# Kernel tuning notes

Hardware: AMD Instinct MI355X
Metric: run time of the kernel (lower is better)

The kernel has to match this reference:

```python
import jax, jax.numpy as jnp
import numpy as np

D_MODEL = 1024
N_HEADS = 16
D_K = D_MODEL // N_HEADS
SCALE = float(np.sqrt(D_K))


def setup_inputs() -> dict:
    key = jax.random.key(0)
    ks = jax.random.split(key, 12)
    B, S = 2, 2048
    std = 1.0 / np.sqrt(D_MODEL)
    inp = {
        "query": jax.random.normal(ks[0], (B, S, D_MODEL), jnp.float32),
        "key": jax.random.normal(ks[1], (B, S, D_MODEL), jnp.float32),
        "value": jax.random.normal(ks[2], (B, S, D_MODEL), jnp.float32),
        "mask": jnp.ones((B, S), jnp.int32),
        "Wq": jax.random.normal(ks[3], (D_MODEL, D_MODEL), jnp.float32) * std,
        "bq": jnp.zeros((D_MODEL,), jnp.float32),
        "Wk": jax.random.normal(ks[4], (D_MODEL, D_MODEL), jnp.float32) * std,
        "bk": jnp.zeros((D_MODEL,), jnp.float32),
        "Wv": jax.random.normal(ks[5], (D_MODEL, D_MODEL), jnp.float32) * std,
        "bv": jnp.zeros((D_MODEL,), jnp.float32),
        "Wo": jax.random.normal(ks[6], (D_MODEL, D_MODEL), jnp.float32) * std,
        "bo": jnp.zeros((D_MODEL,), jnp.float32),
    }
    return inp


def reference(query, key, value, mask, Wq, bq, Wk, bk, Wv, bv, Wo, bo):
    B, S, _ = query.shape
    # projections -> [B, H, S, d_k]
    def proj(x, W, b):
        return (x @ W.T + b).reshape(B, S, N_HEADS, D_K).transpose(0, 2, 1, 3)

    Q = proj(query, Wq, bq)
    K = proj(key, Wk, bk)
    V = proj(value, Wv, bv)
    # [B, H, Sq, Sk] scores
    scores = jnp.einsum("bhqd,bhkd->bhqk", Q, K) / SCALE
    m = mask[:, None, None, :]  # broadcast over heads and query positions
    scores = jnp.where(m == 0, jnp.float32(-1e9), scores)
    attn = jax.nn.softmax(scores, axis=-1)
    # dropout is identity in eval mode
    context = jnp.einsum("bhqk,bhkd->bhqd", attn, V)
    context = context.transpose(0, 2, 1, 3).reshape(B, S, D_MODEL)
    return context @ Wo.T + bo
```

## Files before the change

kernel.cpp:

```cpp
#include <hip/hip_runtime.h>
#include <stdint.h>

#define D_MODEL 1024
#define NH 16
#define DK 64
#define BATCH 2
#define SEQ 2048
#define MROWS (BATCH*SEQ)

typedef float f32x4 __attribute__((ext_vector_type(4)));
typedef __bf16 bf16x8 __attribute__((ext_vector_type(8)));

#define AS1 __attribute__((address_space(1)))
#define AS3 __attribute__((address_space(3)))

#if __has_builtin(__builtin_amdgcn_exp2f)
#define EXP2F(x) __builtin_amdgcn_exp2f(x)
#else
#define EXP2F(x) exp2f(x)
#endif
#if __has_builtin(__builtin_amdgcn_rcpf)
#define RCPF(x) __builtin_amdgcn_rcpf(x)
#else
#define RCPF(x) (1.0f/(x))
#endif

static __device__ __forceinline__ void gld_lds16(const void* g, void* l) {
    __builtin_amdgcn_global_load_lds((const AS1 unsigned int*)g,
                                     (AS3 unsigned int*)l, 16, 0, 0);
}

static __device__ __forceinline__ unsigned short bfbits(float f) {
    return __builtin_bit_cast(unsigned short, (__bf16)f);
}
static __device__ __forceinline__ unsigned int pk2bf(float a, float b) {
    return (unsigned int)bfbits(a) | ((unsigned int)bfbits(b) << 16);
}
static __device__ __forceinline__ float bf2f(unsigned int u) {
    return __builtin_bit_cast(float, u << 16);
}

struct PrepArgs {
    const float* src[7];
    unsigned short* dst[7];
    int n4[7];
};

__global__ __launch_bounds__(256) void prep_cvt(PrepArgs a) {
    const int z = blockIdx.y;
    const float4* s = (const float4*)a.src[z];
    uint2* d = (uint2*)a.dst[z];
    const int n = a.n4[z];
    for (int i = blockIdx.x * blockDim.x + threadIdx.x; i < n;
         i += gridDim.x * blockDim.x) {
        float4 v = s[i];
        uint2 o;
        o.x = pk2bf(v.x, v.y);
        o.y = pk2bf(v.z, v.w);
        d[i] = o;
    }
}

struct GemmArgs {
    const unsigned short* A[3];
    const unsigned short* W[3];
    const float* bias[3];
    void* C[3];
    float scale[3];
    int hm[3];
};

template<bool OUT_F32, int BM, int BN>
__global__ __launch_bounds__(256) void gemm_bt(GemmArgs g) {
    constexpr int IM = BM / 32;
    constexpr int JN = BN / 32;
    __shared__ unsigned short As[BM * 64];
    __shared__ unsigned short Bs[BN * 64];
    const int z = blockIdx.z;
    const char* A = (const char*)g.A[z];
    const char* W = (const char*)g.W[z];
    const float* bias = g.bias[z];
    const float scale = g.scale[z];
    const int hm = g.hm[z];
    const int t = threadIdx.x;
    const int w = t >> 6, lane = t & 63;
    const int m0 = blockIdx.x * BM, n0 = blockIdx.y * BN;
    const int wm = (w >> 1) * (BM / 2), wn = (w & 1) * (BN / 2);

    const int srow = t >> 3;
    const int csw = ((t & 7) * 16) ^ ((srow & 7) << 4);
    const char* pA = A + (size_t)(m0 + srow) * 2048 + csw;
    const char* pW = W + (size_t)(n0 + srow) * 2048 + csw;

    f32x4 acc[IM][JN];
#pragma unroll
    for (int i = 0; i < IM; ++i)
#pragma unroll
        for (int j = 0; j < JN; ++j)
            acc[i][j] = (f32x4){0.f, 0.f, 0.f, 0.f};

    const int g4 = lane >> 4;
    const int kg16 = g4 * 16;
    const int swl = (lane & 7) << 4;

    for (int kt = 0; kt < 16; ++kt) {
        __syncthreads();
#pragma unroll
        for (int p = 0; p < IM; ++p)
            gld_lds16(pA + (size_t)p * (32 * 2048), &As[w * 512 + p * 2048]);
#pragma unroll
        for (int p = 0; p < JN; ++p)
            gld_lds16(pW + (size_t)p * (32 * 2048), &Bs[w * 512 + p * 2048]);
        pA += 128; pW += 128;
        __syncthreads();
#pragma unroll
        for (int ks = 0; ks < 2; ++ks) {
            bf16x8 af[IM], bfv[JN];
#pragma unroll
            for (int i = 0; i < IM; ++i) {
                int ra = wm + i * 16 + (lane & 15);
                af[i] = *(const bf16x8*)((const char*)As + ra * 128 +
                                         ((ks * 64 + kg16) ^ swl));
            }
#pragma unroll
            for (int j = 0; j < JN; ++j) {
                int rb = wn + j * 16 + (lane & 15);
                bfv[j] = *(const bf16x8*)((const char*)Bs + rb * 128 +
                                          ((ks * 64 + kg16) ^ swl));
            }
            __builtin_amdgcn_s_setprio(1);
#pragma unroll
            for (int i = 0; i < IM; ++i)
#pragma unroll
                for (int j = 0; j < JN; ++j)
                    acc[i][j] = __builtin_amdgcn_mfma_f32_16x16x32_bf16(
                        af[i], bfv[j], acc[i][j], 0, 0, 0);
            __builtin_amdgcn_s_setprio(0);
        }
    }

    float bj[JN];
#pragma unroll
    for (int j = 0; j < JN; ++j) bj[j] = bias[n0 + wn + j * 16 + (lane & 15)];

    if (hm == 2) {
#pragma unroll
        for (int i = 0; i < IM; ++i) {
            int row0 = m0 + wm + i * 16 + (g4 << 2);
            int bb = row0 >> 11, ss0 = row0 & 2047;
#pragma unroll
            for (int j = 0; j < JN; ++j) {
                int col = n0 + wn + j * 16 + (lane & 15);
                int hh = col >> 6, dd = col & 63;
                ushort4 o;
                o.x = bfbits(acc[i][j][0] + bj[j]);
                o.y = bfbits(acc[i][j][1] + bj[j]);
                o.z = bfbits(acc[i][j][2] + bj[j]);
                o.w = bfbits(acc[i][j][3] + bj[j]);
                *(ushort4*)((unsigned short*)g.C[z] +
                            (((size_t)(bb * 16 + hh) * 64 + dd) * 2048 + ss0)) = o;
            }
        }
        return;
    }

#pragma unroll
    for (int i = 0; i < IM; ++i)
#pragma unroll
        for (int r = 0; r < 4; ++r) {
            int row = m0 + wm + i * 16 + g4 * 4 + r;
#pragma unroll
            for (int j = 0; j < JN; ++j) {
                int col = n0 + wn + j * 16 + (lane & 15);
                float v = (acc[i][j][r] + bj[j]) * scale;
                if (OUT_F32) {
                    ((float*)g.C[z])[(size_t)row * 1024 + col] = v;
                } else if (hm) {
                    int bb = row >> 11, ss = row & 2047;
                    int hh = col >> 6, dd = col & 63;
                    ((unsigned short*)g.C[z])
                        [(((size_t)(bb * 16 + hh) * 2048) + ss) * 64 + dd] =
                        bfbits(v);
                } else {
                    ((unsigned short*)g.C[z])[(size_t)row * 1024 + col] =
                        bfbits(v);
                }
            }
        }
}

__global__ __launch_bounds__(256) void attn_fwd(
    const unsigned short* __restrict__ Qh,
    const unsigned short* __restrict__ Kh,
    const unsigned short* __restrict__ VtT,
    const int* __restrict__ mask,
    unsigned short* __restrict__ Opart,
    float* __restrict__ Mlf,
    float* __restrict__ Llf) {
    __shared__ unsigned short KlA[4096], KlB[4096];
    __shared__ unsigned short VlA[4096], VlB[4096];
    __shared__ unsigned short Plds[4][2048];
    __shared__ int cfl[4];

    const int wg = blockIdx.x + (int)gridDim.x *
                   (blockIdx.y + (int)gridDim.y * blockIdx.z);
    const int swz = (wg & 7) * 128 + (wg >> 3);
    const int sp = swz & 1, qt = (swz >> 1) & 15, bh = swz >> 5;
    const int b = bh >> 4, h = bh & 15;
    const int kvb = sp * 1024;

    const int t = threadIdx.x, w = t >> 6, lane = t & 63;
    const int wq0 = w * 32;
    const int g = lane >> 4;
    const int kg16 = g * 16;
    const int swl = (lane & 7) << 4;

    const int* mbase = mask + b * SEQ;
    int4 m4 = ((const int4*)(mbase + kvb))[t];
    int myclean = (m4.x != 0) & (m4.y != 0) & (m4.z != 0) & (m4.w != 0);
    int wc = __all(myclean);
    if (lane == 0) cfl[w] = wc;

    const char* Qbase = (const char*)Qh + (size_t)bh * 2048 * 128;
    bf16x8 qf[2][2];
#pragma unroll
    for (int nf = 0; nf < 2; ++nf)
#pragma unroll
        for (int ks = 0; ks < 2; ++ks) {
            int row = qt * 128 + wq0 + nf * 16 + (lane & 15);
            qf[nf][ks] = *(const bf16x8*)(Qbase + (size_t)row * 128 +
                                          ks * 64 + kg16);
        }

    bf16x8 onesf;
#pragma unroll
    for (int j = 0; j < 8; ++j) onesf[j] = (__bf16)1.0f;

    f32x4 cacc[2][4], lacc[2];
#pragma unroll
    for (int i = 0; i < 2; ++i) {
        lacc[i] = (f32x4){0.f, 0.f, 0.f, 0.f};
#pragma unroll
        for (int j = 0; j < 4; ++j) cacc[i][j] = (f32x4){0.f, 0.f, 0.f, 0.f};
    }
    float mstate[2] = {-3e38f, -3e38f};

    const char* Kbyte = (const char*)Kh + (size_t)bh * 2048 * 128;
    const char* Vbyte = (const char*)VtT + (size_t)bh * 64 * 4096;

    const int srow = t >> 3;
    const int csw = ((t & 7) * 16) ^ ((srow & 7) << 4);
    const size_t srow128 = (size_t)srow * 128;
    const size_t srow4096 = (size_t)srow * 4096;

    auto stage = [&](unsigned short* Kd, unsigned short* Vd, int kv0) {
        const char* ks = Kbyte + (size_t)kv0 * 128;
        gld_lds16(ks + srow128 + csw,               Kd + w * 512);
        gld_lds16(ks + srow128 + 32 * 128 + csw,    Kd + 2048 + w * 512);
        const char* vs = Vbyte + (size_t)kv0 * 2;
        gld_lds16(vs + srow4096 + csw,              Vd + w * 512);
        gld_lds16(vs + srow4096 + 32 * 4096 + csw,  Vd + 2048 + w * 512);
    };

    __syncthreads();
    const int clean = cfl[0] & cfl[1] & cfl[2] & cfl[3];

    unsigned short* Pw = &Plds[w][0];

    auto compute = [&](const unsigned short* Kl, const unsigned short* Vl,
                       int kv0) {
        f32x4 sacc[4][2];
#pragma unroll
        for (int i = 0; i < 4; ++i)
#pragma unroll
            for (int j = 0; j < 2; ++j) sacc[i][j] = (f32x4){0.f, 0.f, 0.f, 0.f};
#pragma unroll
        for (int ks = 0; ks < 2; ++ks) {
            bf16x8 kf[4];
#pragma unroll
            for (int mf = 0; mf < 4; ++mf) {
                int r = mf * 16 + (lane & 15);
                kf[mf] = *(const bf16x8*)((const char*)Kl + r * 128 +
                                          ((ks * 64 + kg16) ^ swl));
            }
            __builtin_amdgcn_s_setprio(1);
#pragma unroll
            for (int mf = 0; mf < 4; ++mf)
#pragma unroll
                for (int nf = 0; nf < 2; ++nf)
                    sacc[mf][nf] = __builtin_amdgcn_mfma_f32_16x16x32_bf16(
                        kf[mf], qf[nf][ks], sacc[mf][nf], 0, 0, 0);
            __builtin_amdgcn_s_setprio(0);
        }

        if (!clean) {
#pragma unroll
            for (int mf = 0; mf < 4; ++mf) {
                int4 mk = *(const int4*)(mbase + kv0 + mf * 16 + g * 4);
#pragma unroll
                for (int r = 0; r < 4; ++r) {
                    if ((&mk.x)[r] == 0) {
                        sacc[mf][0][r] = -1e9f;
                        sacc[mf][1][r] = -1e9f;
                    }
                }
            }
        }

        float vm[2];
#pragma unroll
        for (int nf = 0; nf < 2; ++nf) {
            float a0 = fmaxf(fmaxf(sacc[0][nf][0], sacc[0][nf][1]),
                             fmaxf(sacc[0][nf][2], sacc[0][nf][3]));
            float a1 = fmaxf(fmaxf(sacc[1][nf][0], sacc[1][nf][1]),
                             fmaxf(sacc[1][nf][2], sacc[1][nf][3]));
            float a2 = fmaxf(fmaxf(sacc[2][nf][0], sacc[2][nf][1]),
                             fmaxf(sacc[2][nf][2], sacc[2][nf][3]));
            float a3 = fmaxf(fmaxf(sacc[3][nf][0], sacc[3][nf][1]),
                             fmaxf(sacc[3][nf][2], sacc[3][nf][3]));
            float m4x = fmaxf(fmaxf(a0, a1), fmaxf(a2, a3));
            m4x = fmaxf(m4x, __shfl_xor(m4x, 16));
            vm[nf] = fmaxf(m4x, __shfl_xor(m4x, 32));
        }
        if (!__all((vm[0] <= mstate[0] + 8.f) & (vm[1] <= mstate[1] + 8.f))) {
            float sc[2];
#pragma unroll
            for (int nf = 0; nf < 2; ++nf) {
                float mnew = fmaxf(mstate[nf], vm[nf]);
                sc[nf] = EXP2F(mstate[nf] - mnew);
                mstate[nf] = mnew;
            }
#pragma unroll
            for (int mq = 0; mq < 2; ++mq)
#pragma unroll
                for (int r = 0; r < 4; ++r) {
                    float scb = __shfl(sc[mq], g * 4 + r);
                    lacc[mq][r] *= scb;
#pragma unroll
                    for (int nd = 0; nd < 4; ++nd) cacc[mq][nd][r] *= scb;
                }
        }

#pragma unroll
        for (int nf = 0; nf < 2; ++nf) {
            float mn = mstate[nf];
#pragma unroll
            for (int mf = 0; mf < 4; ++mf) {
                unsigned int d0 = pk2bf(EXP2F(sacc[mf][nf][0] - mn),
                                        EXP2F(sacc[mf][nf][1] - mn));
                unsigned int d1 = pk2bf(EXP2F(sacc[mf][nf][2] - mn),
                                        EXP2F(sacc[mf][nf][3] - mn));
                int q = nf * 16 + (lane & 15);
                int kb = mf * 32 + g * 8;
                unsigned long long pv =
                    (unsigned long long)d0 | ((unsigned long long)d1 << 32);
                *(unsigned long long*)((char*)Pw + q * 128 +
                                       (kb ^ ((q & 7) << 4))) = pv;
            }
        }

#pragma unroll
        for (int ks = 0; ks < 2; ++ks) {
            bf16x8 pa[2], vf[4];
#pragma unroll
            for (int mq = 0; mq < 2; ++mq) {
                int r = mq * 16 + (lane & 15);
                pa[mq] = *(const bf16x8*)((const char*)Pw + r * 128 +
                                          ((ks * 64 + kg16) ^ swl));
            }
#pragma unroll
            for (int nd = 0; nd < 4; ++nd) {
                int r = nd * 16 + (lane & 15);
                vf[nd] = *(const bf16x8*)((const char*)Vl + r * 128 +
                                          ((ks * 64 + kg16) ^ swl));
            }
            __builtin_amdgcn_s_setprio(1);
#pragma unroll
            for (int mq = 0; mq < 2; ++mq) {
                lacc[mq] = __builtin_amdgcn_mfma_f32_16x16x32_bf16(
                    pa[mq], onesf, lacc[mq], 0, 0, 0);
#pragma unroll
                for (int nd = 0; nd < 4; ++nd)
                    cacc[mq][nd] = __builtin_amdgcn_mfma_f32_16x16x32_bf16(
                        pa[mq], vf[nd], cacc[mq][nd], 0, 0, 0);
            }
            __builtin_amdgcn_s_setprio(0);
        }
    };

    stage(KlA, VlA, kvb);
    __syncthreads();
    for (int i = 0; i < 8; ++i) {
        const int kv0 = kvb + i * 128;
        stage(KlB, VlB, kv0 + 64);
        compute(KlA, VlA, kv0);
        __syncthreads();
        if (i < 7) stage(KlA, VlA, kv0 + 128);
        compute(KlB, VlB, kv0 + 64);
        __syncthreads();
    }

#pragma unroll
    for (int mq = 0; mq < 2; ++mq)
#pragma unroll
        for (int r = 0; r < 4; ++r) {
            int sq = qt * 128 + wq0 + mq * 16 + g * 4 + r;
            size_t row = (size_t)(sp * 4096 + b * 2048 + sq);
#pragma unroll
            for (int nd = 0; nd < 4; ++nd) {
                int col = h * 64 + nd * 16 + (lane & 15);
                Opart[row * 1024 + col] = bfbits(cacc[mq][nd][r]);
            }
        }
    if ((lane & 15) == 0) {
#pragma unroll
        for (int mq = 0; mq < 2; ++mq)
#pragma unroll
            for (int r = 0; r < 4; ++r)
                Llf[sp * 65536 + bh * 2048 + qt * 128 + wq0 + mq * 16 +
                    g * 4 + r] = lacc[mq][r];
    }
    if (g == 0) {
#pragma unroll
        for (int mq = 0; mq < 2; ++mq)
            Mlf[sp * 65536 + bh * 2048 + qt * 128 + wq0 + mq * 16 +
                (lane & 15)] = mstate[mq];
    }
}

__global__ __launch_bounds__(256) void attn_combine(
    const unsigned short* __restrict__ Op,
    const float* __restrict__ Mlf,
    const float* __restrict__ Llf,
    unsigned short* __restrict__ Cx) {
    const int idx = blockIdx.x * 256 + threadIdx.x;
    const int row = idx >> 7;
    const int c8 = (idx & 127) << 3;
    const int b = row >> 11, s = row & 2047, h = c8 >> 6;
    const int li = (b * 16 + h) * 2048 + s;
    const float m1 = Mlf[li], m2 = Mlf[65536 + li];
    const float l1 = Llf[li], l2 = Llf[65536 + li];
    const float mx = fmaxf(m1, m2);
    float w1 = EXP2F(m1 - mx), w2 = EXP2F(m2 - mx);
    const float inv = RCPF(fmaf(l1, w1, l2 * w2));
    w1 *= inv; w2 *= inv;
    const uint4 o1 = *(const uint4*)(Op + (size_t)row * 1024 + c8);
    const uint4 o2 = *(const uint4*)(Op + (size_t)(4096 + row) * 1024 + c8);
    uint4 o;
    unsigned int rr[4];
#pragma unroll
    for (int j = 0; j < 4; ++j) {
        unsigned int a = ((const unsigned int*)&o1)[j];
        unsigned int c = ((const unsigned int*)&o2)[j];
        float x0 = bf2f(a & 0xffffu) * w1 + bf2f(c & 0xffffu) * w2;
        float x1 = bf2f(a >> 16) * w1 + bf2f(c >> 16) * w2;
        rr[j] = pk2bf(x0, x1);
    }
    o.x = rr[0]; o.y = rr[1]; o.z = rr[2]; o.w = rr[3];
    *(uint4*)(Cx + (size_t)row * 1024 + c8) = o;
}

extern "C" void kernel_launch(void* const* d_in, const int* in_sizes, int n_in,
                              void* d_out, int out_size, void* d_ws, size_t ws_size,
                              hipStream_t stream) {
    const float* q   = (const float*)d_in[0];
    const float* k   = (const float*)d_in[1];
    const float* v   = (const float*)d_in[2];
    const int* mask  = (const int*)d_in[3];
    const float* Wq  = (const float*)d_in[4];
    const float* bq  = (const float*)d_in[5];
    const float* Wk  = (const float*)d_in[6];
    const float* bk  = (const float*)d_in[7];
    const float* Wv  = (const float*)d_in[8];
    const float* bv  = (const float*)d_in[9];
    const float* Wo  = (const float*)d_in[10];
    const float* bo  = (const float*)d_in[11];

    unsigned short* ws = (unsigned short*)d_ws;
    const size_t NX = (size_t)MROWS * D_MODEL;
    const size_t NW = (size_t)D_MODEL * D_MODEL;
    unsigned short* Xq  = ws;
    unsigned short* Xk  = Xq + NX;
    unsigned short* Xv  = Xk + NX;
    unsigned short* Wqb = Xv + NX;
    unsigned short* Wkb = Wqb + NW;
    unsigned short* Wvb = Wkb + NW;
    unsigned short* Wob = Wvb + NW;
    unsigned short* Qhd = Wob + NW;
    unsigned short* Khd = Qhd + NX;
    unsigned short* Vtt = Khd + NX;
    unsigned short* Cx  = Vtt + NX;

    PrepArgs pa;
    pa.src[0] = q;  pa.src[1] = k;  pa.src[2] = v;
    pa.src[3] = Wq; pa.src[4] = Wk; pa.src[5] = Wv; pa.src[6] = Wo;
    pa.dst[0] = Xq;  pa.dst[1] = Xk;  pa.dst[2] = Xv;
    pa.dst[3] = Wqb; pa.dst[4] = Wkb; pa.dst[5] = Wvb; pa.dst[6] = Wob;
    for (int i = 0; i < 3; ++i) pa.n4[i] = (int)(NX / 4);
    for (int i = 3; i < 7; ++i) pa.n4[i] = (int)(NW / 4);
    prep_cvt<<<dim3(256, 7), dim3(256), 0, stream>>>(pa);

    GemmArgs gq;
    gq.A[0] = Xq;  gq.A[1] = Xk;  gq.A[2] = Xv;
    gq.W[0] = Wqb; gq.W[1] = Wkb; gq.W[2] = Wvb;
    gq.bias[0] = bq; gq.bias[1] = bk; gq.bias[2] = bv;
    gq.C[0] = Qhd; gq.C[1] = Khd; gq.C[2] = Vtt;
    gq.scale[0] = 0.125f * 1.44269504088896340736f;
    gq.scale[1] = 1.f; gq.scale[2] = 1.f;
    gq.hm[0] = 1; gq.hm[1] = 1; gq.hm[2] = 2;
    gemm_bt<false, 128, 128><<<dim3(32, 8, 3), dim3(256), 0, stream>>>(gq);

    unsigned short* Opart = Xq;
    float* Mlf = (float*)Xv;
    float* Llf = Mlf + 2 * 65536;
    attn_fwd<<<dim3(16, 32, 2), dim3(256), 0, stream>>>(
        Qhd, Khd, Vtt, mask, Opart, Mlf, Llf);

    attn_combine<<<dim3(2048), dim3(256), 0, stream>>>(Opart, Mlf, Llf, Cx);

    GemmArgs go;
    go.A[0] = Cx; go.W[0] = Wob; go.bias[0] = bo; go.C[0] = d_out;
    go.scale[0] = 1.f; go.hm[0] = 0;
    go.A[1] = go.A[2] = nullptr; go.W[1] = go.W[2] = nullptr;
    go.bias[1] = go.bias[2] = nullptr; go.C[1] = go.C[2] = nullptr;
    go.scale[1] = go.scale[2] = 1.f; go.hm[1] = go.hm[2] = 0;
    gemm_bt<true, 64, 128><<<dim3(64, 8, 1), dim3(256), 0, stream>>>(go);
}
```

Baseline: 244.1 us.

## Load K/V fragments directly from global memory in attention, drop LDS double buffer

The attention kernel no longer stages K and V tiles into double-buffered shared memory with barriers. Each wave now reads its MFMA operand fragments straight from global memory (relying on L1/L2 reuse across the four waves), and the mask-clean check becomes per-wave with no shared flag or sync. Launch bounds ask for 4 blocks per CU to raise occupancy now that LDS use is smaller. The output projection GEMM tile shape also changes from 64x128 to 128x64. The trade-off is more redundant global/cache traffic and uncoalesced V fragment loads in exchange for removing barriers and LDS pressure.

```diff
diff --git a/kernel.cpp b/kernel.cpp
--- a/kernel.cpp
+++ b/kernel.cpp
@@ -189,7 +189,7 @@
         }
 }
 
-__global__ __launch_bounds__(256) void attn_fwd(
+__global__ __launch_bounds__(256, 4) void attn_fwd(
     const unsigned short* __restrict__ Qh,
     const unsigned short* __restrict__ Kh,
     const unsigned short* __restrict__ VtT,
@@ -197,10 +197,7 @@
     unsigned short* __restrict__ Opart,
     float* __restrict__ Mlf,
     float* __restrict__ Llf) {
-    __shared__ unsigned short KlA[4096], KlB[4096];
-    __shared__ unsigned short VlA[4096], VlB[4096];
     __shared__ unsigned short Plds[4][2048];
-    __shared__ int cfl[4];
 
     const int wg = blockIdx.x + (int)gridDim.x *
                    (blockIdx.y + (int)gridDim.y * blockIdx.z);
@@ -216,12 +213,15 @@
     const int swl = (lane & 7) << 4;
 
     const int* mbase = mask + b * SEQ;
-    int4 m4 = ((const int4*)(mbase + kvb))[t];
-    int myclean = (m4.x != 0) & (m4.y != 0) & (m4.z != 0) & (m4.w != 0);
-    int wc = __all(myclean);
-    if (lane == 0) cfl[w] = wc;
-
-    const char* Qbase = (const char*)Qh + (size_t)bh * 2048 * 128;
+    int myclean = 1;
+#pragma unroll
+    for (int i = 0; i < 4; ++i) {
+        int4 m4 = ((const int4*)(mbase + kvb))[lane + 64 * i];
+        myclean &= (m4.x != 0) & (m4.y != 0) & (m4.z != 0) & (m4.w != 0);
+    }
+    const int clean = (int)__all(myclean);
+
+    const char* Qbase = (const char*)Qh + (size_t)bh * (2048 * 128);
     bf16x8 qf[2][2];
 #pragma unroll
     for (int nf = 0; nf < 2; ++nf)
@@ -245,30 +245,15 @@
     }
     float mstate[2] = {-3e38f, -3e38f};
 
-    const char* Kbyte = (const char*)Kh + (size_t)bh * 2048 * 128;
-    const char* Vbyte = (const char*)VtT + (size_t)bh * 64 * 4096;
-
-    const int srow = t >> 3;
-    const int csw = ((t & 7) * 16) ^ ((srow & 7) << 4);
-    const size_t srow128 = (size_t)srow * 128;
-    const size_t srow4096 = (size_t)srow * 4096;
-
-    auto stage = [&](unsigned short* Kd, unsigned short* Vd, int kv0) {
-        const char* ks = Kbyte + (size_t)kv0 * 128;
-        gld_lds16(ks + srow128 + csw,               Kd + w * 512);
-        gld_lds16(ks + srow128 + 32 * 128 + csw,    Kd + 2048 + w * 512);
-        const char* vs = Vbyte + (size_t)kv0 * 2;
-        gld_lds16(vs + srow4096 + csw,              Vd + w * 512);
-        gld_lds16(vs + srow4096 + 32 * 4096 + csw,  Vd + 2048 + w * 512);
-    };
-
-    __syncthreads();
-    const int clean = cfl[0] & cfl[1] & cfl[2] & cfl[3];
+    const char* Kbyte = (const char*)Kh + (size_t)bh * (2048 * 128);
+    const char* Vbyte = (const char*)VtT + (size_t)bh * (64 * 4096);
 
     unsigned short* Pw = &Plds[w][0];
 
-    auto compute = [&](const unsigned short* Kl, const unsigned short* Vl,
-                       int kv0) {
+#pragma unroll 2
+    for (int it = 0; it < 16; ++it) {
+        const int kv0 = kvb + it * 64;
+
         f32x4 sacc[4][2];
 #pragma unroll
         for (int i = 0; i < 4; ++i)
@@ -278,11 +263,10 @@
         for (int ks = 0; ks < 2; ++ks) {
             bf16x8 kf[4];
 #pragma unroll
-            for (int mf = 0; mf < 4; ++mf) {
-                int r = mf * 16 + (lane & 15);
-                kf[mf] = *(const bf16x8*)((const char*)Kl + r * 128 +
-                                          ((ks * 64 + kg16) ^ swl));
-            }
+            for (int mf = 0; mf < 4; ++mf)
+                kf[mf] = *(const bf16x8*)(Kbyte +
+                    (size_t)(kv0 + mf * 16 + (lane & 15)) * 128 +
+                    ks * 64 + kg16);
             __builtin_amdgcn_s_setprio(1);
 #pragma unroll
             for (int mf = 0; mf < 4; ++mf)
@@ -369,11 +353,10 @@
                                           ((ks * 64 + kg16) ^ swl));
             }
 #pragma unroll
-            for (int nd = 0; nd < 4; ++nd) {
-                int r = nd * 16 + (lane & 15);
-                vf[nd] = *(const bf16x8*)((const char*)Vl + r * 128 +
-                                          ((ks * 64 + kg16) ^ swl));
-            }
+            for (int nd = 0; nd < 4; ++nd)
+                vf[nd] = *(const bf16x8*)(Vbyte +
+                    (size_t)(nd * 16 + (lane & 15)) * 4096 +
+                    (size_t)(kv0 + ks * 32 + g * 8) * 2);
             __builtin_amdgcn_s_setprio(1);
 #pragma unroll
             for (int mq = 0; mq < 2; ++mq) {
@@ -386,18 +369,6 @@
             }
             __builtin_amdgcn_s_setprio(0);
         }
-    };
-
-    stage(KlA, VlA, kvb);
-    __syncthreads();
-    for (int i = 0; i < 8; ++i) {
-        const int kv0 = kvb + i * 128;
-        stage(KlB, VlB, kv0 + 64);
-        compute(KlA, VlA, kv0);
-        __syncthreads();
-        if (i < 7) stage(KlA, VlA, kv0 + 128);
-        compute(KlB, VlB, kv0 + 64);
-        __syncthreads();
     }
 
 #pragma unroll
@@ -524,5 +495,5 @@
     go.A[1] = go.A[2] = nullptr; go.W[1] = go.W[2] = nullptr;
     go.bias[1] = go.bias[2] = nullptr; go.C[1] = go.C[2] = nullptr;
     go.scale[1] = go.scale[2] = 1.f; go.hm[1] = go.hm[2] = 0;
-    gemm_bt<true, 64, 128><<<dim3(64, 8, 1), dim3(256), 0, stream>>>(go);
-}
+    gemm_bt<true, 128, 64><<<dim3(32, 16, 1), dim3(256), 0, stream>>>(go);
+}
```

After: 333.2 us. 1.37x slower.
